# Optimization experiments

Measured on AMD Instinct MI355X. Metric: run time of the kernel, lower is better.

Reference implementation:

```python
import jax, jax.numpy as jnp
import numpy as np

B, T, DEMO, V, NMOD = 64, 4096, 8, 1, 15
NPOS = 16                      # n_positional_dims
PHI_IN = NPOS + V + NMOD       # 32
PHI_W, LAT = 128, 128
PSI_W, PSI_LAT = 128, 128
DP, H = 64, 4                  # dot_prod_dim, n_heads
RHO_W, OUT = 128, 1
MAX_TIMESCALE = 100.0


def _he(k, din, dout):
    return jax.random.normal(k, (din, dout), jnp.float32) * np.sqrt(2.0 / din)


def setup_inputs() -> dict:
    key = jax.random.key(0)
    ks = jax.random.split(key, 24)
    inp = {
        'demo': jax.random.normal(ks[0], (B, DEMO), jnp.float32),
        'times': jax.random.uniform(ks[1], (B, T, 1), jnp.float32) * 100.0,
        'values': jax.random.normal(ks[2], (B, T, V), jnp.float32),
        'measurements': jax.random.randint(ks[3], (B, T), 0, NMOD),
        'lengths': jax.random.randint(ks[4], (B,), 1, T),
    }
    i = [5]
    def nd(din, dout):
        w = _he(ks[i[0]], din, dout); i[0] += 1
        return w, jnp.zeros((dout,), jnp.float32)
    p = {}
    p['demo_w1'], p['demo_b1'] = nd(DEMO, PHI_W)
    p['demo_w2'], p['demo_b2'] = nd(PHI_W, PHI_IN)
    p['phi_w1'], p['phi_b1'] = nd(PHI_IN, PHI_W)
    p['phi_w2'], p['phi_b2'] = nd(PHI_W, PHI_W)
    p['phi_w3'], p['phi_b3'] = nd(PHI_W, LAT)
    p['psi_w1'], p['psi_b1'] = nd(PHI_IN, PSI_W)
    p['psi_w2'], p['psi_b2'] = nd(PSI_W, PSI_W)
    p['psi_w3'], p['psi_b3'] = nd(PSI_W, PSI_LAT)
    p['rho_attn_w'], p['rho_attn_b'] = nd(PSI_LAT, LAT)
    p['W_k'] = _he(ks[i[0]], PHI_IN + LAT, DP * H); i[0] += 1
    p['W_q'] = jax.random.normal(ks[i[0]], (H, DP), jnp.float32) * 0.02; i[0] += 1
    p['rho_w1'], p['rho_b1'] = nd(H * LAT, RHO_W)
    p['rho_w2'], p['rho_b2'] = nd(RHO_W, RHO_W)
    p['rho_w3'], p['rho_b3'] = nd(RHO_W, OUT)
    inp.update(p)
    return inp


def reference(demo, times, values, measurements, lengths,
              demo_w1, demo_b1, demo_w2, demo_b2,
              phi_w1, phi_b1, phi_w2, phi_b2, phi_w3, phi_b3,
              psi_w1, psi_b1, psi_w2, psi_b2, psi_w3, psi_b3,
              rho_attn_w, rho_attn_b, W_k, W_q,
              rho_w1, rho_b1, rho_w2, rho_b2, rho_w3, rho_b3):
    relu = jax.nn.relu
    # positional encoding of observation times  [B,T,NPOS]
    timescales = MAX_TIMESCALE ** jnp.linspace(0.0, 1.0, NPOS // 2).astype(times.dtype)
    scaled = times / timescales[None, None, :]
    tt = jnp.concatenate([jnp.sin(scaled), jnp.cos(scaled)], axis=-1)
    onehot = jax.nn.one_hot(measurements, NMOD, dtype=tt.dtype)
    combined = jnp.concatenate([tt, values, onehot], axis=-1)        # [B,T,PHI_IN]
    # demographics encoder -> extra set element prepended per batch
    demo_enc = relu(demo @ demo_w1 + demo_b1) @ demo_w2 + demo_b2    # [B,PHI_IN]
    x = jnp.concatenate([demo_enc[:, None, :], combined], axis=1)    # [B,T+1,PHI_IN]
    mask = jnp.arange(T + 1)[None, :] < (lengths + 1)[:, None]       # [B,T+1]
    maskf = mask.astype(x.dtype)
    # phi network  [B,T+1,LAT]
    enc = relu(relu(relu(x @ phi_w1 + phi_b1) @ phi_w2 + phi_b2) @ phi_w3 + phi_b3)
    # attention psi network + segment (masked) mean
    psi = relu(relu(relu(x @ psi_w1 + psi_b1) @ psi_w2 + psi_b2) @ psi_w3 + psi_b3)
    cnt = jnp.sum(maskf, axis=1, keepdims=True)                      # [B,1]
    agg = jnp.sum(psi * maskf[..., None], axis=1) / cnt              # [B,PSI_LAT]
    agg = relu(agg @ rho_attn_w + rho_attn_b)                        # [B,LAT]
    comb = jnp.concatenate(
        [x, jnp.broadcast_to(agg[:, None, :], (B, T + 1, LAT))], axis=-1)
    keys = (comb @ W_k).reshape(B, T + 1, H, DP)
    preattn = jnp.einsum('bthd,hd->bth', keys, W_q) / jnp.sqrt(jnp.asarray(DP, x.dtype))
    preattn = jnp.where(mask[..., None], preattn, -1e9)
    attn = jax.nn.softmax(preattn, axis=1)                           # segment softmax [B,T+1,H]
    # per-head weighted segment sum, heads concatenated
    head_agg = jnp.einsum('bth,btl->bhl', attn, enc * maskf[..., None])
    feat = head_agg.reshape(B, H * LAT)
    out = relu(relu(feat @ rho_w1 + rho_b1) @ rho_w2 + rho_b2) @ rho_w3 + rho_b3
    return jax.nn.sigmoid(out)
```

## Files before the change

### kernel.cpp

```cpp
#include <hip/hip_runtime.h>
#include <hip/hip_bf16.h>
#include <math.h>

#define TT     4096
#define NWG    768
#define PREC   516
#define NB     64

typedef short s16x8 __attribute__((ext_vector_type(8)));
typedef float f32x4 __attribute__((ext_vector_type(4)));

__device__ __constant__ float INV_TS[8] = {
    1.0f,                 0.5179474679231213f, 0.2682695795279726f, 0.1389495494373138f,
    0.0719685673001152f,  0.0372759372031494f, 0.0193069772888325f, 0.01f };

__device__ __forceinline__ ushort f2bf(float f) {
    uint u = __float_as_uint(f);
    return (ushort)((u + 0x7fffu + ((u >> 16) & 1u)) >> 16);
}
__device__ __forceinline__ float bf2f(ushort h) {
    return __uint_as_float(((uint)h) << 16);
}
__device__ __forceinline__ uint pkbf(float a, float b) {
    union { __hip_bfloat162 h; uint u; } cv;
    cv.h = __float22bfloat162_rn(make_float2(a, b));
    return cv.u;
}
__device__ __forceinline__ int hswz(int m, int col) {
    return ((((col >> 3) - 2 * (m & 7)) & 15) << 3) | (col & 7);
}
#define PIN_A(v) asm volatile("" : "+a"(v))

__global__ __launch_bounds__(128) void prep_all(
    const float* __restrict__ demo,
    const float* __restrict__ dw1, const float* __restrict__ db1,
    const float* __restrict__ dw2, const float* __restrict__ db2,
    const float* __restrict__ W_k, const float* __restrict__ W_q,
    const float* __restrict__ w1, const float* __restrict__ w2,
    const float* __restrict__ w3,
    float* __restrict__ demo_enc, float* __restrict__ w_eff,
    ushort* __restrict__ ws16, float* __restrict__ partials)
{
    const int b = blockIdx.x, tid = threadIdx.x;
    if (b < NB) {
        for (int j = tid; j < PREC; j += 128) partials[b*PREC + j] = 0.f;
        __shared__ float h[128];
        float a = db1[tid];
#pragma unroll
        for (int k = 0; k < 8; k++) a += demo[b*8 + k] * dw1[k*128 + tid];
        h[tid] = fmaxf(a, 0.f);
        __syncthreads();
        if (tid < 32) {
            float e = db2[tid];
#pragma unroll 8
            for (int k = 0; k < 128; k++) e += h[k] * dw2[k*32 + tid];
            demo_enc[b*32 + tid] = e;
        }
    } else if (b == NB) {
        const int f = tid >> 2, hh = tid & 3;
        float s = 0.f;
#pragma unroll 8
        for (int d = 0; d < 64; d++) s += W_k[f*256 + hh*64 + d] * W_q[hh*64 + d];
        w_eff[f*4 + hh] = s * 0.125f;
    } else {
        ushort* w1T = ws16;
        ushort* w2T = ws16 + 4096;
        ushort* w3T = ws16 + 20480;
        const int n = (b - 65) & 127, which = (b - 65) >> 7, k = tid;
        if (which == 0)      w2T[n*128 + k] = f2bf(w2[k*128 + n]);
        else if (which == 1) w3T[n*128 + k] = f2bf(w3[k*128 + n]);
        else if (k < 32)     w1T[n*32  + k] = f2bf(w1[k*128 + n]);
    }
}

__global__ void __launch_bounds__(256)
__attribute__((amdgpu_waves_per_eu(3, 3)))
fused_main(
    const float* __restrict__ times,  const float* __restrict__ values,
    const int*   __restrict__ meas,   const int*   __restrict__ lengths,
    const float* __restrict__ demo_enc, const float* __restrict__ w_eff,
    const ushort* __restrict__ wT16,
    const float* __restrict__ b1, const float* __restrict__ b2,
    const float* __restrict__ b3,
    float* __restrict__ partials)
{
    const ushort* w1T = wT16;
    const ushort* w2T = wT16 + 4096;
    const ushort* w3T = wT16 + 20480;

    __shared__ __align__(16) char arena[51968];
    ushort (*Hhi )[136]    = (ushort(*)[136])(arena);
    ushort (*encT)[88]     = (ushort(*)[88]) (arena);
    ushort (*H2  )[136]    = (ushort(*)[136])(arena + 22528);
    ushort (*Xhi )[40]     = (ushort(*)[40]) (arena + 39936);
    float  (*spart)[4][64] = (float(*)[4][64])(arena + 45056);
    ushort (*wexpT)[88]    = (ushort(*)[88]) (arena + 49152);

    const int tid  = threadIdx.x;
    const int lane = tid & 63, wav = tid >> 6;
    const int l15  = lane & 15, q = lane >> 4;
    const int nb0  = wav * 32;
    const int t    = lane;

    for (int i = tid; i < 12*88/2; i += 256) ((uint*)&wexpT[4][0])[i] = 0u;

    s16x8 ah1[2];    f32x4 bv1[2];
    s16x8 ah2[2][4]; f32x4 bv2[2];
    s16x8 wb3[2][4]; float b3l[2];
#pragma unroll
    for (int nt = 0; nt < 2; nt++) {
        const int np = nb0 + nt*16 + l15;
        ah1[nt] = *(const s16x8*)(w1T + np*32 + q*8);
        bv1[nt] = *(const f32x4*)(b1 + nb0 + nt*16 + q*4);
#pragma unroll
        for (int ks = 0; ks < 4; ks++) {
            ah2[nt][ks] = *(const s16x8*)(w2T + np*128 + ks*32 + q*8);
            wb3[nt][ks] = *(const s16x8*)(w3T + np*128 + ks*32 + q*8);
        }
        bv2[nt] = *(const f32x4*)(b2 + nb0 + nt*16 + q*4);
        b3l[nt] = b3[np];
    }

    const int wg = blockIdx.x;
    const int start = wg*5 + ((wg < 256) ? wg : 256);
    const int cnt   = 5 + (wg < 256 ? 1 : 0);
    int b = start >> 6, tile = start & 63;

    f32x4 hacc[2] = {{0.f,0.f,0.f,0.f},{0.f,0.f,0.f,0.f}};
    float zacc = 0.f;

    float pf_tm = 0.f, pf_vl = 0.f; int pf_mm = -1;
    {
        const int gt = tile*64 + t;
        if (gt >= 1) {
            const int ti = b*TT + gt - 1;
            pf_tm = times[ti]; pf_vl = values[ti]; pf_mm = meas[ti];
        }
    }

#pragma unroll 1
    for (int i = 0; i < cnt; i++) {
        PIN_A(ah1[0]); PIN_A(ah1[1]);
#pragma unroll
        for (int nt = 0; nt < 2; nt++)
#pragma unroll
            for (int ks = 0; ks < 4; ks++) { PIN_A(ah2[nt][ks]); PIN_A(wb3[nt][ks]); }
        PIN_A(hacc[0]); PIN_A(hacc[1]);

        const int gt  = tile*64 + t;
        const int len = lengths[b];
        const bool last = (i == cnt - 1);
        const int bn = b + (tile == 63), tilen = (tile + 1) & 63;

        float x[8];
        if (gt == 0) {
#pragma unroll
            for (int j = 0; j < 8; j++) x[j] = demo_enc[b*32 + wav*8 + j];
        } else {
            if (wav == 0) {
#pragma unroll
                for (int j = 0; j < 8; j++) x[j] = __sinf(pf_tm * INV_TS[j]);
            } else if (wav == 1) {
#pragma unroll
                for (int j = 0; j < 8; j++) x[j] = __cosf(pf_tm * INV_TS[j]);
            } else if (wav == 2) {
                x[0] = pf_vl;
#pragma unroll
                for (int j = 1; j < 8; j++) x[j] = (pf_mm == j-1) ? 1.f : 0.f;
            } else {
#pragma unroll
                for (int j = 0; j < 8; j++) x[j] = (pf_mm == 7+j) ? 1.f : 0.f;
            }
        }
        {
            float s0 = 0, s1 = 0, s2 = 0, s3 = 0;
#pragma unroll
            for (int j = 0; j < 8; j++) {
                const float* we = w_eff + (wav*8 + j)*4;
                s0 += x[j]*we[0]; s1 += x[j]*we[1]; s2 += x[j]*we[2]; s3 += x[j]*we[3];
            }
            spart[wav][0][t] = s0; spart[wav][1][t] = s1;
            spart[wav][2][t] = s2; spart[wav][3][t] = s3;
        }
        {
            uint4 uh = {pkbf(x[0],x[1]), pkbf(x[2],x[3]), pkbf(x[4],x[5]), pkbf(x[6],x[7])};
            *(uint4*)&Xhi[t][wav*8] = uh;
        }
        if (!last) {
            const int gt2 = tilen*64 + t;
            if (gt2 >= 1) {
                const int ti = bn*TT + gt2 - 1;
                pf_tm = times[ti]; pf_vl = values[ti]; pf_mm = meas[ti];
            } else { pf_mm = -1; }
        }
        __syncthreads();
        {
            float ss = spart[0][wav][t] + spart[1][wav][t]
                     + spart[2][wav][t] + spart[3][wav][t];
            float wxf = (gt <= len) ? __expf(ss) : 0.f;
            ushort w16 = (ushort)(pkbf(wxf, wxf) & 0xffffu);
            wexpT[wav][t] = w16;
            zacc += bf2f(w16);
        }

#pragma unroll
        for (int tt = 0; tt < 4; tt++) {
            const int m = tt*16 + l15;
            s16x8 bh = *(const s16x8*)&Xhi[m][q*8];
#pragma unroll
            for (int nt = 0; nt < 2; nt++) {
                f32x4 acc = {0.f, 0.f, 0.f, 0.f};
                acc = __builtin_amdgcn_mfma_f32_16x16x32_bf16(ah1[nt], bh, acc, 0, 0, 0);
                uint2 uh = {pkbf(fmaxf(acc[0]+bv1[nt][0],0.f), fmaxf(acc[1]+bv1[nt][1],0.f)),
                            pkbf(fmaxf(acc[2]+bv1[nt][2],0.f), fmaxf(acc[3]+bv1[nt][3],0.f))};
                *(uint2*)&Hhi[m][hswz(m, nb0 + nt*16 + q*4)] = uh;
            }
        }
        __syncthreads();

#pragma unroll
        for (int tt = 0; tt < 4; tt++) {
            const int m = tt*16 + l15;
            s16x8 bh[4];
#pragma unroll
            for (int ks = 0; ks < 4; ks++)
                bh[ks] = *(const s16x8*)&Hhi[m][hswz(m, ks*32 + q*8)];
#pragma unroll
            for (int nt = 0; nt < 2; nt++) {
                f32x4 acc = {0.f, 0.f, 0.f, 0.f};
#pragma unroll
                for (int ks = 0; ks < 4; ks++)
                    acc = __builtin_amdgcn_mfma_f32_16x16x32_bf16(ah2[nt][ks], bh[ks], acc, 0, 0, 0);
                uint2 uh = {pkbf(fmaxf(acc[0]+bv2[nt][0],0.f), fmaxf(acc[1]+bv2[nt][1],0.f)),
                            pkbf(fmaxf(acc[2]+bv2[nt][2],0.f), fmaxf(acc[3]+bv2[nt][3],0.f))};
                *(uint2*)&H2[m][hswz(m, nb0 + nt*16 + q*4)] = uh;
            }
        }
        __syncthreads();

#pragma unroll
        for (int tt = 0; tt < 4; tt++) {
            const int m = tt*16 + l15;
            s16x8 a3[4];
#pragma unroll
            for (int ks = 0; ks < 4; ks++)
                a3[ks] = *(const s16x8*)&H2[m][hswz(m, ks*32 + q*8)];
#pragma unroll
            for (int nt = 0; nt < 2; nt++) {
                f32x4 acc = {0.f,0.f,0.f,0.f};
#pragma unroll
                for (int ks = 0; ks < 4; ks++)
                    acc = __builtin_amdgcn_mfma_f32_16x16x32_bf16(a3[ks], wb3[nt][ks], acc, 0, 0, 0);
                uint2 uh = {pkbf(fmaxf(acc[0]+b3l[nt],0.f), fmaxf(acc[1]+b3l[nt],0.f)),
                            pkbf(fmaxf(acc[2]+b3l[nt],0.f), fmaxf(acc[3]+b3l[nt],0.f))};
                *(uint2*)&encT[nb0 + nt*16 + l15][tt*16 + q*4] = uh;
            }
        }

        {
            s16x8 af0 = *(const s16x8*)&wexpT[l15][q*8];
            s16x8 af1 = *(const s16x8*)&wexpT[l15][32 + q*8];
#pragma unroll
            for (int nt = 0; nt < 2; nt++) {
                const ushort* erow = &encT[nb0 + nt*16 + l15][0];
                hacc[nt] = __builtin_amdgcn_mfma_f32_16x16x32_bf16(
                               af0, *(const s16x8*)(erow + q*8), hacc[nt], 0, 0, 0);
                hacc[nt] = __builtin_amdgcn_mfma_f32_16x16x32_bf16(
                               af1, *(const s16x8*)(erow + 32 + q*8), hacc[nt], 0, 0, 0);
            }
        }

        if (tile == 63 || last) {
            float* outp = partials + (size_t)b * PREC;
            if (q == 0) {
#pragma unroll
                for (int nt = 0; nt < 2; nt++)
#pragma unroll
                    for (int r = 0; r < 4; r++)
                        atomicAdd(&outp[r*128 + nb0 + nt*16 + l15], hacc[nt][r]);
            }
            float z = zacc;
#pragma unroll
            for (int mask = 1; mask <= 32; mask <<= 1) z += __shfl_xor(z, mask);
            if (lane == 0) atomicAdd(&outp[512 + wav], z);
            hacc[0] = f32x4{0.f,0.f,0.f,0.f};
            hacc[1] = f32x4{0.f,0.f,0.f,0.f};
            zacc = 0.f;
        }
        b = bn; tile = tilen;
    }
}

__global__ __launch_bounds__(512) void final_kernel(
    const float* __restrict__ partials,
    const float* __restrict__ rw1, const float* __restrict__ rb1,
    const float* __restrict__ rw2, const float* __restrict__ rb2,
    const float* __restrict__ rw3, const float* __restrict__ rb3,
    float* __restrict__ out)
{
    const int b = blockIdx.x, tid = threadIdx.x;
    const int n = tid & 127, h = tid >> 7;
    __shared__ float feat[512];
    __shared__ float p[4][128];
    __shared__ float r1s[128];
    __shared__ float r2s[128];
    __shared__ float zsh[4];
    const float* pb = partials + (size_t)b * PREC;
    if (tid < 4) zsh[tid] = pb[512 + tid];
    __syncthreads();
    feat[tid] = pb[tid] / zsh[tid >> 7];
    __syncthreads();

    {
        float a = 0.f;
        const float* w = rw1 + h*128*128 + n;
        const float* f = feat + h*128;
#pragma unroll 16
        for (int k = 0; k < 128; k++) a += f[k] * w[k*128];
        p[h][n] = a;
    }
    __syncthreads();
    if (h == 0) r1s[n] = fmaxf(p[0][n] + p[1][n] + p[2][n] + p[3][n] + rb1[n], 0.f);
    __syncthreads();

    {
        float a = 0.f;
        const float* w = rw2 + h*32*128 + n;
        const float* f = r1s + h*32;
#pragma unroll 16
        for (int k = 0; k < 32; k++) a += f[k] * w[k*128];
        p[h][n] = a;
    }
    __syncthreads();
    if (h == 0) r2s[n] = fmaxf(p[0][n] + p[1][n] + p[2][n] + p[3][n] + rb2[n], 0.f);
    __syncthreads();

    if (tid < 64) {
        float v = r2s[tid] * rw3[tid] + r2s[tid + 64] * rw3[tid + 64];
#pragma unroll
        for (int mask = 1; mask <= 32; mask <<= 1) v += __shfl_xor(v, mask);
        if (tid == 0) out[b] = 1.f / (1.f + expf(-(v + rb3[0])));
    }
}

extern "C" void kernel_launch(void* const* d_in, const int* in_sizes, int n_in,
                              void* d_out, int out_size, void* d_ws, size_t ws_size,
                              hipStream_t stream) {
    const float* demo    = (const float*)d_in[0];
    const float* times   = (const float*)d_in[1];
    const float* values  = (const float*)d_in[2];
    const int*   meas    = (const int*)  d_in[3];
    const int*   lengths = (const int*)  d_in[4];
    const float* demo_w1 = (const float*)d_in[5];
    const float* demo_b1 = (const float*)d_in[6];
    const float* demo_w2 = (const float*)d_in[7];
    const float* demo_b2 = (const float*)d_in[8];
    const float* phi_w1  = (const float*)d_in[9];
    const float* phi_b1  = (const float*)d_in[10];
    const float* phi_w2  = (const float*)d_in[11];
    const float* phi_b2  = (const float*)d_in[12];
    const float* phi_w3  = (const float*)d_in[13];
    const float* phi_b3  = (const float*)d_in[14];
    const float* W_k     = (const float*)d_in[23];
    const float* W_q     = (const float*)d_in[24];
    const float* rho_w1  = (const float*)d_in[25];
    const float* rho_b1  = (const float*)d_in[26];
    const float* rho_w2  = (const float*)d_in[27];
    const float* rho_b2  = (const float*)d_in[28];
    const float* rho_w3  = (const float*)d_in[29];
    const float* rho_b3  = (const float*)d_in[30];

    float*  ws       = (float*)d_ws;
    float*  demo_enc = ws;
    float*  w_eff    = ws + 2048;
    ushort* wT16     = (ushort*)(ws + 2176);
    float*  partials = ws + 20608;

    prep_all<<<449, 128, 0, stream>>>(demo, demo_w1, demo_b1, demo_w2, demo_b2,
                                      W_k, W_q, phi_w1, phi_w2, phi_w3,
                                      demo_enc, w_eff, wT16, partials);
    fused_main<<<NWG, 256, 0, stream>>>(
        times, values, meas, lengths, demo_enc, w_eff, wT16,
        phi_b1, phi_b2, phi_b3, partials);
    final_kernel<<<NB, 512, 0, stream>>>(partials, rho_w1, rho_b1, rho_w2, rho_b2,
                                         rho_w3, rho_b3, (float*)d_out);
}
```

Before: 160.8 us.

## Split token featurization into a separate kernel writing bf16 features to global memory

Moves the per-token work (sin/cos positional encoding, one-hot construction, attention-logit dot product) out of the fused MLP kernel into a new featurize kernel. That kernel writes bf16 feature rows and fp32 logits to a workspace buffer. The main kernel then loads its MFMA B operands straight from global memory, which drops the Xhi/spart LDS staging and its prefetch registers and shrinks the LDS footprint. In exchange it adds a kernel launch and a global round trip of roughly 17 MB for features plus 4 MB for logits.

```diff
diff --git a/kernel.cpp b/kernel.cpp
--- a/kernel.cpp
+++ b/kernel.cpp
@@ -6,6 +6,7 @@
 #define NWG    768
 #define PREC   516
 #define NB     64
+#define GTOK   4160
 
 typedef short s16x8 __attribute__((ext_vector_type(8)));
 typedef float f32x4 __attribute__((ext_vector_type(4)));
@@ -73,12 +74,71 @@
     }
 }
 
+__global__ __launch_bounds__(256) void featurize(
+    const float* __restrict__ times,  const float* __restrict__ values,
+    const int*   __restrict__ meas,
+    const float* __restrict__ demo_enc, const float* __restrict__ w_eff,
+    ushort* __restrict__ Xbf,
+    float*  __restrict__ slog)
+{
+    __shared__ float spart[4][4][64];
+    const int b = blockIdx.y, tile = blockIdx.x;
+    const int tid = threadIdx.x, t = tid & 63, g = tid >> 6;
+    const int gt = tile*64 + t;
+
+    float x[8];
+    if (gt == 0) {
+#pragma unroll
+        for (int j = 0; j < 8; j++) x[j] = demo_enc[b*32 + g*8 + j];
+    } else if (gt <= TT) {
+        const int ti = b*TT + gt - 1;
+        if (g == 0) {
+            float tm = times[ti];
+#pragma unroll
+            for (int j = 0; j < 8; j++) x[j] = __sinf(tm * INV_TS[j]);
+        } else if (g == 1) {
+            float tm = times[ti];
+#pragma unroll
+            for (int j = 0; j < 8; j++) x[j] = __cosf(tm * INV_TS[j]);
+        } else if (g == 2) {
+            int mm = meas[ti]; x[0] = values[ti];
+#pragma unroll
+            for (int j = 1; j < 8; j++) x[j] = (mm == j-1) ? 1.f : 0.f;
+        } else {
+            int mm = meas[ti];
+#pragma unroll
+            for (int j = 0; j < 8; j++) x[j] = (mm == 7+j) ? 1.f : 0.f;
+        }
+    } else {
+#pragma unroll
+        for (int j = 0; j < 8; j++) x[j] = 0.f;
+    }
+    {
+        float s0 = 0, s1 = 0, s2 = 0, s3 = 0;
+#pragma unroll
+        for (int j = 0; j < 8; j++) {
+            const float* we = w_eff + (g*8 + j)*4;
+            s0 += x[j]*we[0]; s1 += x[j]*we[1]; s2 += x[j]*we[2]; s3 += x[j]*we[3];
+        }
+        spart[g][0][t] = s0; spart[g][1][t] = s1;
+        spart[g][2][t] = s2; spart[g][3][t] = s3;
+    }
+    {
+        uint4 uh = {pkbf(x[0],x[1]), pkbf(x[2],x[3]), pkbf(x[4],x[5]), pkbf(x[6],x[7])};
+        *(uint4*)&Xbf[((size_t)b*GTOK + gt)*32 + g*8] = uh;
+    }
+    __syncthreads();
+    {
+        float ss = spart[0][g][t] + spart[1][g][t] + spart[2][g][t] + spart[3][g][t];
+        slog[((size_t)b*GTOK + gt)*4 + g] = ss;
+    }
+}
+
 __global__ void __launch_bounds__(256)
 __attribute__((amdgpu_waves_per_eu(3, 3)))
 fused_main(
-    const float* __restrict__ times,  const float* __restrict__ values,
-    const int*   __restrict__ meas,   const int*   __restrict__ lengths,
-    const float* __restrict__ demo_enc, const float* __restrict__ w_eff,
+    const int*    __restrict__ lengths,
+    const ushort* __restrict__ Xbf,   const float* __restrict__ slog,
     const ushort* __restrict__ wT16,
     const float* __restrict__ b1, const float* __restrict__ b2,
     const float* __restrict__ b3,
@@ -88,13 +148,11 @@
     const ushort* w2T = wT16 + 4096;
     const ushort* w3T = wT16 + 20480;
 
-    __shared__ __align__(16) char arena[51968];
+    __shared__ __align__(16) char arena[43776];
     ushort (*Hhi )[136]    = (ushort(*)[136])(arena);
     ushort (*encT)[88]     = (ushort(*)[88]) (arena);
     ushort (*H2  )[136]    = (ushort(*)[136])(arena + 22528);
-    ushort (*Xhi )[40]     = (ushort(*)[40]) (arena + 39936);
-    float  (*spart)[4][64] = (float(*)[4][64])(arena + 45056);
-    ushort (*wexpT)[88]    = (ushort(*)[88]) (arena + 49152);
+    ushort (*wexpT)[88]    = (ushort(*)[88]) (arena + 40960);
 
     const int tid  = threadIdx.x;
     const int lane = tid & 63, wav = tid >> 6;
@@ -129,15 +187,6 @@
     f32x4 hacc[2] = {{0.f,0.f,0.f,0.f},{0.f,0.f,0.f,0.f}};
     float zacc = 0.f;
 
-    float pf_tm = 0.f, pf_vl = 0.f; int pf_mm = -1;
-    {
-        const int gt = tile*64 + t;
-        if (gt >= 1) {
-            const int ti = b*TT + gt - 1;
-            pf_tm = times[ti]; pf_vl = values[ti]; pf_mm = meas[ti];
-        }
-    }
-
 #pragma unroll 1
     for (int i = 0; i < cnt; i++) {
         PIN_A(ah1[0]); PIN_A(ah1[1]);
@@ -152,52 +201,16 @@
         const bool last = (i == cnt - 1);
         const int bn = b + (tile == 63), tilen = (tile + 1) & 63;
 
-        float x[8];
-        if (gt == 0) {
-#pragma unroll
-            for (int j = 0; j < 8; j++) x[j] = demo_enc[b*32 + wav*8 + j];
-        } else {
-            if (wav == 0) {
-#pragma unroll
-                for (int j = 0; j < 8; j++) x[j] = __sinf(pf_tm * INV_TS[j]);
-            } else if (wav == 1) {
-#pragma unroll
-                for (int j = 0; j < 8; j++) x[j] = __cosf(pf_tm * INV_TS[j]);
-            } else if (wav == 2) {
-                x[0] = pf_vl;
-#pragma unroll
-                for (int j = 1; j < 8; j++) x[j] = (pf_mm == j-1) ? 1.f : 0.f;
-            } else {
-#pragma unroll
-                for (int j = 0; j < 8; j++) x[j] = (pf_mm == 7+j) ? 1.f : 0.f;
-            }
-        }
-        {
-            float s0 = 0, s1 = 0, s2 = 0, s3 = 0;
-#pragma unroll
-            for (int j = 0; j < 8; j++) {
-                const float* we = w_eff + (wav*8 + j)*4;
-                s0 += x[j]*we[0]; s1 += x[j]*we[1]; s2 += x[j]*we[2]; s3 += x[j]*we[3];
-            }
-            spart[wav][0][t] = s0; spart[wav][1][t] = s1;
-            spart[wav][2][t] = s2; spart[wav][3][t] = s3;
-        }
-        {
-            uint4 uh = {pkbf(x[0],x[1]), pkbf(x[2],x[3]), pkbf(x[4],x[5]), pkbf(x[6],x[7])};
-            *(uint4*)&Xhi[t][wav*8] = uh;
-        }
-        if (!last) {
-            const int gt2 = tilen*64 + t;
-            if (gt2 >= 1) {
-                const int ti = bn*TT + gt2 - 1;
-                pf_tm = times[ti]; pf_vl = values[ti]; pf_mm = meas[ti];
-            } else { pf_mm = -1; }
-        }
+        const ushort* xb = Xbf + ((size_t)b*GTOK + tile*64)*32;
+        s16x8 xf[4];
+#pragma unroll
+        for (int tt = 0; tt < 4; tt++)
+            xf[tt] = *(const s16x8*)(xb + (tt*16 + l15)*32 + q*8);
+        float sl = slog[((size_t)b*GTOK + gt)*4 + wav];
+
         __syncthreads();
         {
-            float ss = spart[0][wav][t] + spart[1][wav][t]
-                     + spart[2][wav][t] + spart[3][wav][t];
-            float wxf = (gt <= len) ? __expf(ss) : 0.f;
+            float wxf = (gt <= len) ? __expf(sl) : 0.f;
             ushort w16 = (ushort)(pkbf(wxf, wxf) & 0xffffu);
             wexpT[wav][t] = w16;
             zacc += bf2f(w16);
@@ -206,7 +219,7 @@
 #pragma unroll
         for (int tt = 0; tt < 4; tt++) {
             const int m = tt*16 + l15;
-            s16x8 bh = *(const s16x8*)&Xhi[m][q*8];
+            s16x8 bh = xf[tt];
 #pragma unroll
             for (int nt = 0; nt < 2; nt++) {
                 f32x4 acc = {0.f, 0.f, 0.f, 0.f};
@@ -375,13 +388,16 @@
     float*  w_eff    = ws + 2048;
     ushort* wT16     = (ushort*)(ws + 2176);
     float*  partials = ws + 20608;
+    ushort* Xbf      = (ushort*)(ws + 53632);
+    float*  slog     = ws + 53632 + 4259840;
 
     prep_all<<<449, 128, 0, stream>>>(demo, demo_w1, demo_b1, demo_w2, demo_b2,
                                       W_k, W_q, phi_w1, phi_w2, phi_w3,
                                       demo_enc, w_eff, wT16, partials);
+    featurize<<<dim3(65, NB), 256, 0, stream>>>(times, values, meas,
+                                                demo_enc, w_eff, Xbf, slog);
     fused_main<<<NWG, 256, 0, stream>>>(
-        times, values, meas, lengths, demo_enc, w_eff, wT16,
-        phi_b1, phi_b2, phi_b3, partials);
+        lengths, Xbf, slog, wT16, phi_b1, phi_b2, phi_b3, partials);
     final_kernel<<<NB, 512, 0, stream>>>(partials, rho_w1, rho_b1, rho_w2, rho_b2,
                                          rho_w3, rho_b3, (float*)d_out);
 }
```

After: 175.1 us. +8.9%, slower.
